# Kernel optimization log

Measured on AMD Instinct MI355X. Metric: run time of the kernel, lower is better.

Reference implementation:

```python
import jax, jax.numpy as jnp
import numpy as np

N_PREV = 8191
DIMS = 4096


def setup_inputs() -> dict:
    key = jax.random.key(0)
    k1, k2, k3, k4, k5 = jax.random.split(key, 5)
    prev_inps = jax.random.normal(k1, (N_PREV, DIMS), dtype=jnp.float32)
    inp = jax.random.normal(k2, (DIMS,), dtype=jnp.float32)
    # learned parameters, init std=0.01 as in the torch module
    W_Q = jax.random.normal(k3, (DIMS, DIMS), dtype=jnp.float32) * 0.01
    W_K = jax.random.normal(k4, (DIMS, DIMS), dtype=jnp.float32) * 0.01
    W_V = jax.random.normal(k5, (DIMS, DIMS), dtype=jnp.float32) * 0.01
    return {"prev_inps": prev_inps, "inp": inp, "W_Q": W_Q, "W_K": W_K, "W_V": W_V}


def reference(prev_inps, inp, W_Q, W_K, W_V):
    # One masked self-attention decode step.
    inputs = jnp.concatenate([prev_inps, inp[None, :]], axis=0)  # (n+1, d)
    query = W_Q @ inp                                            # (d,)
    keys = jnp.einsum('md,nd->nm', W_K, inputs)                  # (n+1, d)
    values = jnp.einsum('md,nd->nm', W_V, inputs)                # (n+1, d)
    logits = keys @ query                                        # (n+1,)
    aweights = jax.nn.softmax(logits, axis=-1)                   # (n+1,)
    context = aweights @ values                                  # (d,)
    output = context + inp                                       # residual
    return (output, inputs)
```

## Files before the change

kernel.cpp:

```cpp
#include <hip/hip_runtime.h>
#include <math.h>

#define D      4096
#define NPREV  8191
#define NROWS  8192

typedef float f4 __attribute__((ext_vector_type(4)));

static __device__ __forceinline__ f4 nt_load4(const float* p) {
    return __builtin_nontemporal_load(reinterpret_cast<const f4*>(p));
}
static __device__ __forceinline__ void nt_store4(f4 v, float* p) {
    __builtin_nontemporal_store(v, reinterpret_cast<f4*>(p));
}
static __device__ __forceinline__ f4 ld4(const float* p) {
    return *reinterpret_cast<const f4*>(p);
}
static __device__ __forceinline__ void st4(f4 v, float* p) {
    *reinterpret_cast<f4*>(p) = v;
}

template<bool RESIDUAL>
__global__ void k_matvec_rows(const float* __restrict__ W, const float* __restrict__ v,
                              const float* __restrict__ resid, float* __restrict__ out) {
    int row  = blockIdx.x * 4 + (threadIdx.x >> 6);
    int lane = threadIdx.x & 63;
    const float* Wrow = W + (size_t)row * D;
    float acc = 0.f;
    #pragma unroll
    for (int i = 0; i < 16; ++i) {
        int c = lane + i * 64;
        f4 w = nt_load4(Wrow + 4 * c);
        f4 x = ld4(v + 4 * c);
        acc += w.x * x.x + w.y * x.y + w.z * x.z + w.w * x.w;
    }
    #pragma unroll
    for (int off = 32; off; off >>= 1) acc += __shfl_down(acc, off, 64);
    if (lane == 0) out[row] = RESIDUAL ? (acc + resid[row]) : acc;
}

#define NCH 64
__global__ void k_colvec_partial(const float* __restrict__ W, const float* __restrict__ q,
                                 float* __restrict__ part) {
    int d4 = blockIdx.x * 256 + threadIdx.x;
    int m0 = blockIdx.y * (D / NCH);
    f4 acc = (f4)0.f;
    #pragma unroll 4
    for (int r = 0; r < D / NCH; ++r) {
        float qm = q[m0 + r];
        acc += qm * nt_load4(W + (size_t)(m0 + r) * D + 4 * d4);
    }
    st4(acc, part + (size_t)blockIdx.y * D + 4 * d4);
}

__global__ void k_kq_reduce(const float* __restrict__ part, float* __restrict__ kq) {
    __shared__ float s[4][64];
    int b = blockIdx.x;
    int cg = threadIdx.x >> 6, l = threadIdx.x & 63;
    float acc = 0.f;
    #pragma unroll
    for (int i = 0; i < NCH / 4; ++i)
        acc += part[(size_t)(cg * (NCH / 4) + i) * D + b * 64 + l];
    s[cg][l] = acc;
    __syncthreads();
    if (cg == 0) kq[b * 64 + l] = s[0][l] + s[1][l] + s[2][l] + s[3][l];
}

#define FB   512
#define FR   (NROWS / FB)
__global__ __launch_bounds__(1024, 4) void k_flash(
        const float* __restrict__ prev, const float* __restrict__ inp,
        const float* __restrict__ kq, float* __restrict__ io,
        float* __restrict__ ms, float* __restrict__ ctxpart) {
    __shared__ float s_wred[16][FR];
    __shared__ float s_log[FR];
    const int n0 = blockIdx.x * FR;
    const int t = threadIdx.x;
    const int wid = t >> 6, lane = t & 63;
    const f4 kqv = ld4(kq + 4 * t);

    f4 x[FR];
    #pragma unroll
    for (int r = 0; r < FR; ++r) {
        int n = n0 + r;
        const float* src = (n < NPREV) ? (prev + (size_t)n * D) : inp;
        x[r] = nt_load4(src + 4 * t);
    }
    float p[FR];
    #pragma unroll
    for (int r = 0; r < FR; ++r) {
        int n = n0 + r;
        nt_store4(x[r], io + (size_t)n * D + 4 * t);
        p[r] = x[r].x * kqv.x + x[r].y * kqv.y + x[r].z * kqv.z + x[r].w * kqv.w;
    }
    #pragma unroll
    for (int r = 0; r < FR; ++r) {
        float v = p[r];
        #pragma unroll
        for (int off = 32; off; off >>= 1) v += __shfl_down(v, off, 64);
        if (lane == 0) s_wred[wid][r] = v;
    }
    __syncthreads();
    if (t < FR) {
        float s = 0.f;
        #pragma unroll
        for (int w = 0; w < 16; ++w) s += s_wred[w][t];
        s_log[t] = s;
    }
    __syncthreads();
    float m_b = -INFINITY;
    #pragma unroll
    for (int r = 0; r < FR; ++r) m_b = fmaxf(m_b, s_log[r]);
    float e[FR], s_b = 0.f;
    #pragma unroll
    for (int r = 0; r < FR; ++r) { e[r] = __expf(s_log[r] - m_b); s_b += e[r]; }
    f4 a = (f4)0.f;
    #pragma unroll
    for (int r = 0; r < FR; ++r) a += e[r] * x[r];
    st4(a, ctxpart + (size_t)blockIdx.x * D + 4 * t);
    if (t == 0) { ms[2 * blockIdx.x] = m_b; ms[2 * blockIdx.x + 1] = s_b; }
}

#define NGRP 32
#define GSZ  (FB / NGRP)
__global__ void k_combine1(const float* __restrict__ ms, const float* __restrict__ ctxpart,
                           float* __restrict__ ctx2, float* __restrict__ msg) {
    __shared__ float sm[2 * GSZ];
    int t = threadIdx.x, g = blockIdx.y;
    if (t < 2 * GSZ) sm[t] = ms[2 * GSZ * g + t];
    __syncthreads();
    float Mg = -INFINITY;
    #pragma unroll
    for (int i = 0; i < GSZ; ++i) Mg = fmaxf(Mg, sm[2 * i]);
    float Sg = 0.f;
    #pragma unroll
    for (int i = 0; i < GSZ; ++i) Sg += sm[2 * i + 1] * __expf(sm[2 * i] - Mg);
    int d4 = blockIdx.x * 256 + t;
    f4 a = (f4)0.f;
    #pragma unroll
    for (int i = 0; i < GSZ; ++i) {
        int b = GSZ * g + i;
        a += __expf(sm[2 * i] - Mg) * ld4(ctxpart + (size_t)b * D + 4 * d4);
    }
    st4(a, ctx2 + (size_t)g * D + 4 * d4);
    if (blockIdx.x == 0 && t == 0) { msg[2 * g] = Mg; msg[2 * g + 1] = Sg; }
}

__global__ void k_combine2(const float* __restrict__ msg, const float* __restrict__ ctx2,
                           float* __restrict__ ctx) {
    __shared__ float sm[2 * NGRP];
    int t = threadIdx.x;
    if (t < 2 * NGRP) sm[t] = msg[t];
    __syncthreads();
    float M = -INFINITY;
    #pragma unroll
    for (int g = 0; g < NGRP; ++g) M = fmaxf(M, sm[2 * g]);
    float S = 0.f;
    #pragma unroll
    for (int g = 0; g < NGRP; ++g) S += sm[2 * g + 1] * __expf(sm[2 * g] - M);
    int d4 = blockIdx.x * 256 + t;
    f4 a = (f4)0.f;
    #pragma unroll
    for (int g = 0; g < NGRP; ++g)
        a += __expf(sm[2 * g] - M) * ld4(ctx2 + (size_t)g * D + 4 * d4);
    st4(a * (1.f / S), ctx + 4 * d4);
}

extern "C" void kernel_launch(void* const* d_in, const int* in_sizes, int n_in,
                              void* d_out, int out_size, void* d_ws, size_t ws_size,
                              hipStream_t stream) {
    const float* prev = (const float*)d_in[0];
    const float* inp  = (const float*)d_in[1];
    const float* W_Q  = (const float*)d_in[2];
    const float* W_K  = (const float*)d_in[3];
    const float* W_V  = (const float*)d_in[4];
    float* out = (float*)d_out;
    float* io  = out + D;
    float* ws  = (float*)d_ws;

    float* q       = ws;
    float* kq      = q + D;
    float* part    = kq + D;
    float* ms      = part + (size_t)NCH * D;
    float* ctxpart = ms + 2 * FB;
    float* ctx2    = ctxpart + (size_t)FB * D;
    float* msg     = ctx2 + (size_t)NGRP * D;
    float* ctx     = msg + 2 * NGRP;

    k_matvec_rows<false><<<1024, 256, 0, stream>>>(W_Q, inp, nullptr, q);
    k_colvec_partial<<<dim3(4, NCH), 256, 0, stream>>>(W_K, q, part);
    k_kq_reduce<<<64, 256, 0, stream>>>(part, kq);
    k_flash<<<FB, 1024, 0, stream>>>(prev, inp, kq, io, ms, ctxpart);
    k_combine1<<<dim3(4, NGRP), 256, 0, stream>>>(ms, ctxpart, ctx2, msg);
    k_combine2<<<4, 256, 0, stream>>>(msg, ctx2, ctx);
    k_matvec_rows<true><<<1024, 256, 0, stream>>>(W_V, ctx, inp, out);
}
```

Before: 121.3 us.

## Fuse reductions into producer kernels via last-block atomic counters

The separate kq reduction kernel is folded into the column-matvec kernel, and the first softmax combine stage is folded into the flash kernel. In each case the last block to finish a group, found with an atomic counter after a threadfence, does the reduction. This removes two kernel launches and their inter-kernel gaps, in exchange for a memset launch, fences and atomics, and a serialized tail where only the last block per group does the reduce.

```diff
diff --git a/kernel.cpp b/kernel.cpp
--- a/kernel.cpp
+++ b/kernel.cpp
@@ -4,6 +4,11 @@
 #define D      4096
 #define NPREV  8191
 #define NROWS  8192
+#define FB     512
+#define FR     (NROWS / FB)
+#define NGRP   32
+#define GSZ    (FB / NGRP)
+#define NCH    64
 
 typedef float f4 __attribute__((ext_vector_type(4)));
 
@@ -39,42 +44,43 @@
     if (lane == 0) out[row] = RESIDUAL ? (acc + resid[row]) : acc;
 }
 
-#define NCH 64
-__global__ void k_colvec_partial(const float* __restrict__ W, const float* __restrict__ q,
-                                 float* __restrict__ part) {
-    int d4 = blockIdx.x * 256 + threadIdx.x;
-    int m0 = blockIdx.y * (D / NCH);
+__global__ void k_kq_fused(const float* __restrict__ W, const float* __restrict__ q,
+                           float* part, float* kq, unsigned int* cnt) {
+    __shared__ int s_flag;
+    int t = threadIdx.x;
+    int s = blockIdx.x;
+    int c = blockIdx.y;
+    int d4 = s * 256 + t;
+    int m0 = c * (D / NCH);
     f4 acc = (f4)0.f;
     #pragma unroll 4
-    for (int r = 0; r < D / NCH; ++r) {
-        float qm = q[m0 + r];
-        acc += qm * nt_load4(W + (size_t)(m0 + r) * D + 4 * d4);
-    }
-    st4(acc, part + (size_t)blockIdx.y * D + 4 * d4);
-}
-
-__global__ void k_kq_reduce(const float* __restrict__ part, float* __restrict__ kq) {
-    __shared__ float s[4][64];
-    int b = blockIdx.x;
-    int cg = threadIdx.x >> 6, l = threadIdx.x & 63;
-    float acc = 0.f;
-    #pragma unroll
-    for (int i = 0; i < NCH / 4; ++i)
-        acc += part[(size_t)(cg * (NCH / 4) + i) * D + b * 64 + l];
-    s[cg][l] = acc;
-    __syncthreads();
-    if (cg == 0) kq[b * 64 + l] = s[0][l] + s[1][l] + s[2][l] + s[3][l];
-}
-
-#define FB   512
-#define FR   (NROWS / FB)
+    for (int r = 0; r < D / NCH; ++r)
+        acc += q[m0 + r] * nt_load4(W + (size_t)(m0 + r) * D + 4 * d4);
+    st4(acc, part + (size_t)c * D + 4 * d4);
+    __threadfence();
+    __syncthreads();
+    if (t == 0) s_flag = (atomicAdd(&cnt[s], 1u) == NCH - 1);
+    __syncthreads();
+    if (s_flag) {
+        __threadfence();
+        f4 a = (f4)0.f;
+        #pragma unroll 8
+        for (int cc = 0; cc < NCH; ++cc)
+            a += ld4(part + (size_t)cc * D + 4 * d4);
+        st4(a, kq + 4 * d4);
+    }
+}
+
 __global__ __launch_bounds__(1024, 4) void k_flash(
         const float* __restrict__ prev, const float* __restrict__ inp,
         const float* __restrict__ kq, float* __restrict__ io,
-        float* __restrict__ ms, float* __restrict__ ctxpart) {
+        float* ms, float* ctxpart, float* ctx2, float* msg, unsigned int* cnt) {
     __shared__ float s_wred[16][FR];
     __shared__ float s_log[FR];
-    const int n0 = blockIdx.x * FR;
+    __shared__ float s_gms[2 * GSZ];
+    __shared__ int s_flag;
+    const int bid = blockIdx.x;
+    const int n0 = bid * FR;
     const int t = threadIdx.x;
     const int wid = t >> 6, lane = t & 63;
     const f4 kqv = ld4(kq + 4 * t);
@@ -117,33 +123,33 @@
     f4 a = (f4)0.f;
     #pragma unroll
     for (int r = 0; r < FR; ++r) a += e[r] * x[r];
-    st4(a, ctxpart + (size_t)blockIdx.x * D + 4 * t);
-    if (t == 0) { ms[2 * blockIdx.x] = m_b; ms[2 * blockIdx.x + 1] = s_b; }
-}
-
-#define NGRP 32
-#define GSZ  (FB / NGRP)
-__global__ void k_combine1(const float* __restrict__ ms, const float* __restrict__ ctxpart,
-                           float* __restrict__ ctx2, float* __restrict__ msg) {
-    __shared__ float sm[2 * GSZ];
-    int t = threadIdx.x, g = blockIdx.y;
-    if (t < 2 * GSZ) sm[t] = ms[2 * GSZ * g + t];
-    __syncthreads();
-    float Mg = -INFINITY;
-    #pragma unroll
-    for (int i = 0; i < GSZ; ++i) Mg = fmaxf(Mg, sm[2 * i]);
-    float Sg = 0.f;
-    #pragma unroll
-    for (int i = 0; i < GSZ; ++i) Sg += sm[2 * i + 1] * __expf(sm[2 * i] - Mg);
-    int d4 = blockIdx.x * 256 + t;
-    f4 a = (f4)0.f;
-    #pragma unroll
-    for (int i = 0; i < GSZ; ++i) {
-        int b = GSZ * g + i;
-        a += __expf(sm[2 * i] - Mg) * ld4(ctxpart + (size_t)b * D + 4 * d4);
-    }
-    st4(a, ctx2 + (size_t)g * D + 4 * d4);
-    if (blockIdx.x == 0 && t == 0) { msg[2 * g] = Mg; msg[2 * g + 1] = Sg; }
+    st4(a, ctxpart + (size_t)bid * D + 4 * t);
+    if (t == 0) { ms[2 * bid] = m_b; ms[2 * bid + 1] = s_b; }
+
+    const int g = bid / GSZ;
+    __threadfence();
+    __syncthreads();
+    if (t == 0) s_flag = (atomicAdd(&cnt[g], 1u) == GSZ - 1);
+    __syncthreads();
+    if (s_flag) {
+        __threadfence();
+        if (t < 2 * GSZ) s_gms[t] = ms[2 * GSZ * g + t];
+        __syncthreads();
+        float Mg = -INFINITY;
+        #pragma unroll
+        for (int i = 0; i < GSZ; ++i) Mg = fmaxf(Mg, s_gms[2 * i]);
+        float Sg = 0.f;
+        #pragma unroll
+        for (int i = 0; i < GSZ; ++i) Sg += s_gms[2 * i + 1] * __expf(s_gms[2 * i] - Mg);
+        f4 ga = (f4)0.f;
+        #pragma unroll
+        for (int i = 0; i < GSZ; ++i) {
+            int b = GSZ * g + i;
+            ga += __expf(s_gms[2 * i] - Mg) * ld4(ctxpart + (size_t)b * D + 4 * t);
+        }
+        st4(ga, ctx2 + (size_t)g * D + 4 * t);
+        if (t == 0) { msg[2 * g] = Mg; msg[2 * g + 1] = Sg; }
+    }
 }
 
 __global__ void k_combine2(const float* __restrict__ msg, const float* __restrict__ ctx2,
@@ -186,12 +192,14 @@
     float* ctx2    = ctxpart + (size_t)FB * D;
     float* msg     = ctx2 + (size_t)NGRP * D;
     float* ctx     = msg + 2 * NGRP;
+    unsigned int* cnt_kq    = (unsigned int*)(ctx + D);
+    unsigned int* cnt_flash = cnt_kq + 4;
+
+    hipMemsetAsync(cnt_kq, 0, (4 + NGRP) * sizeof(unsigned int), stream);
 
     k_matvec_rows<false><<<1024, 256, 0, stream>>>(W_Q, inp, nullptr, q);
-    k_colvec_partial<<<dim3(4, NCH), 256, 0, stream>>>(W_K, q, part);
-    k_kq_reduce<<<64, 256, 0, stream>>>(part, kq);
-    k_flash<<<FB, 1024, 0, stream>>>(prev, inp, kq, io, ms, ctxpart);
-    k_combine1<<<dim3(4, NGRP), 256, 0, stream>>>(ms, ctxpart, ctx2, msg);
+    k_kq_fused<<<dim3(4, NCH), 256, 0, stream>>>(W_K, q, part, kq, cnt_kq);
+    k_flash<<<FB, 1024, 0, stream>>>(prev, inp, kq, io, ms, ctxpart, ctx2, msg, cnt_flash);
     k_combine2<<<4, 256, 0, stream>>>(msg, ctx2, ctx);
     k_matvec_rows<true><<<1024, 256, 0, stream>>>(W_V, ctx, inp, out);
 }
```

Result: slower. 433.3 us (+257.2%).

## Fuse K^T q reduction and softmax combine stages into single kernels

Applied to the files above, without the earlier changes.

Replaces the two-kernel K^T·q computation (partial chunks plus a global reduce) with one kernel that stages q in shared memory and reduces across 64 row groups inside the block. The two-level softmax combine is merged into one kernel that computes the global max and sum per block and then weights all 512 partial contexts. Prev input loads in the flash kernel switch from nontemporal to regular loads. The aim is fewer launches and less intermediate global traffic. The cost is lower parallelism: 256 blocks for kq and 32 blocks for combine.

```diff
diff --git a/kernel.cpp b/kernel.cpp
--- a/kernel.cpp
+++ b/kernel.cpp
@@ -4,6 +4,8 @@
 #define D      4096
 #define NPREV  8191
 #define NROWS  8192
+#define FB     512
+#define FR     (NROWS / FB)
 
 typedef float f4 __attribute__((ext_vector_type(4)));
 
@@ -39,35 +41,32 @@
     if (lane == 0) out[row] = RESIDUAL ? (acc + resid[row]) : acc;
 }
 
-#define NCH 64
-__global__ void k_colvec_partial(const float* __restrict__ W, const float* __restrict__ q,
-                                 float* __restrict__ part) {
-    int d4 = blockIdx.x * 256 + threadIdx.x;
-    int m0 = blockIdx.y * (D / NCH);
+__global__ void k_kq(const float* __restrict__ W, const float* __restrict__ q,
+                     float* __restrict__ kq) {
+    __shared__ float s_q[D];
+    __shared__ f4 s_part[64][4];
+    int t = threadIdx.x;
+    int b = blockIdx.x;
+    for (int i = t; i < D; i += 256) s_q[i] = q[i];
+    __syncthreads();
+    int c4 = b * 4 + (t & 3);
+    int r0 = t >> 2;
     f4 acc = (f4)0.f;
-    #pragma unroll 4
-    for (int r = 0; r < D / NCH; ++r) {
-        float qm = q[m0 + r];
-        acc += qm * nt_load4(W + (size_t)(m0 + r) * D + 4 * d4);
+    #pragma unroll 16
+    for (int i = 0; i < 64; ++i) {
+        int m = r0 + i * 64;
+        acc += s_q[m] * nt_load4(W + (size_t)m * D + 4 * c4);
     }
-    st4(acc, part + (size_t)blockIdx.y * D + 4 * d4);
+    s_part[r0][t & 3] = acc;
+    __syncthreads();
+    if (t < 4) {
+        f4 a = (f4)0.f;
+        #pragma unroll
+        for (int g = 0; g < 64; ++g) a += s_part[g][t];
+        st4(a, kq + 4 * (b * 4 + t));
+    }
 }
 
-__global__ void k_kq_reduce(const float* __restrict__ part, float* __restrict__ kq) {
-    __shared__ float s[4][64];
-    int b = blockIdx.x;
-    int cg = threadIdx.x >> 6, l = threadIdx.x & 63;
-    float acc = 0.f;
-    #pragma unroll
-    for (int i = 0; i < NCH / 4; ++i)
-        acc += part[(size_t)(cg * (NCH / 4) + i) * D + b * 64 + l];
-    s[cg][l] = acc;
-    __syncthreads();
-    if (cg == 0) kq[b * 64 + l] = s[0][l] + s[1][l] + s[2][l] + s[3][l];
-}
-
-#define FB   512
-#define FR   (NROWS / FB)
 __global__ __launch_bounds__(1024, 4) void k_flash(
         const float* __restrict__ prev, const float* __restrict__ inp,
         const float* __restrict__ kq, float* __restrict__ io,
@@ -84,7 +83,7 @@
     for (int r = 0; r < FR; ++r) {
         int n = n0 + r;
         const float* src = (n < NPREV) ? (prev + (size_t)n * D) : inp;
-        x[r] = nt_load4(src + 4 * t);
+        x[r] = ld4(src + 4 * t);
     }
     float p[FR];
     #pragma unroll
@@ -121,49 +120,45 @@
     if (t == 0) { ms[2 * blockIdx.x] = m_b; ms[2 * blockIdx.x + 1] = s_b; }
 }
 
-#define NGRP 32
-#define GSZ  (FB / NGRP)
-__global__ void k_combine1(const float* __restrict__ ms, const float* __restrict__ ctxpart,
-                           float* __restrict__ ctx2, float* __restrict__ msg) {
-    __shared__ float sm[2 * GSZ];
-    int t = threadIdx.x, g = blockIdx.y;
-    if (t < 2 * GSZ) sm[t] = ms[2 * GSZ * g + t];
+__global__ void k_combine(const float* __restrict__ ms, const float* __restrict__ ctxpart,
+                          float* __restrict__ ctx) {
+    __shared__ float s_w[FB];
+    __shared__ float s_red[12];
+    __shared__ f4 s_acc[8][32];
+    int t = threadIdx.x;
+    int lane = t & 63, wid = t >> 6;
+    float m0 = ms[2 * t], m1 = ms[2 * (t + 256)];
+    float mx = fmaxf(m0, m1);
+    #pragma unroll
+    for (int off = 32; off; off >>= 1) mx = fmaxf(mx, __shfl_down(mx, off, 64));
+    if (lane == 0) s_red[wid] = mx;
     __syncthreads();
-    float Mg = -INFINITY;
+    float M = fmaxf(fmaxf(s_red[0], s_red[1]), fmaxf(s_red[2], s_red[3]));
+    float w0 = __expf(m0 - M), w1 = __expf(m1 - M);
+    s_w[t] = w0; s_w[t + 256] = w1;
+    float sc = w0 * ms[2 * t + 1] + w1 * ms[2 * (t + 256) + 1];
     #pragma unroll
-    for (int i = 0; i < GSZ; ++i) Mg = fmaxf(Mg, sm[2 * i]);
-    float Sg = 0.f;
-    #pragma unroll
-    for (int i = 0; i < GSZ; ++i) Sg += sm[2 * i + 1] * __expf(sm[2 * i] - Mg);
-    int d4 = blockIdx.x * 256 + t;
+    for (int off = 32; off; off >>= 1) sc += __shfl_down(sc, off, 64);
+    if (lane == 0) s_red[8 + wid] = sc;
+    __syncthreads();
+    float S = s_red[8] + s_red[9] + s_red[10] + s_red[11];
+    int c  = t & 31;
+    int g8 = t >> 5;
+    int col4 = blockIdx.x * 32 + c;
     f4 a = (f4)0.f;
-    #pragma unroll
-    for (int i = 0; i < GSZ; ++i) {
-        int b = GSZ * g + i;
-        a += __expf(sm[2 * i] - Mg) * ld4(ctxpart + (size_t)b * D + 4 * d4);
+    #pragma unroll 8
+    for (int i = 0; i < 64; ++i) {
+        int p = g8 * 64 + i;
+        a += s_w[p] * ld4(ctxpart + (size_t)p * D + 4 * col4);
     }
-    st4(a, ctx2 + (size_t)g * D + 4 * d4);
-    if (blockIdx.x == 0 && t == 0) { msg[2 * g] = Mg; msg[2 * g + 1] = Sg; }
-}
-
-__global__ void k_combine2(const float* __restrict__ msg, const float* __restrict__ ctx2,
-                           float* __restrict__ ctx) {
-    __shared__ float sm[2 * NGRP];
-    int t = threadIdx.x;
-    if (t < 2 * NGRP) sm[t] = msg[t];
+    s_acc[g8][c] = a;
     __syncthreads();
-    float M = -INFINITY;
-    #pragma unroll
-    for (int g = 0; g < NGRP; ++g) M = fmaxf(M, sm[2 * g]);
-    float S = 0.f;
-    #pragma unroll
-    for (int g = 0; g < NGRP; ++g) S += sm[2 * g + 1] * __expf(sm[2 * g] - M);
-    int d4 = blockIdx.x * 256 + t;
-    f4 a = (f4)0.f;
-    #pragma unroll
-    for (int g = 0; g < NGRP; ++g)
-        a += __expf(sm[2 * g] - M) * ld4(ctx2 + (size_t)g * D + 4 * d4);
-    st4(a * (1.f / S), ctx + 4 * d4);
+    if (t < 32) {
+        f4 aa = (f4)0.f;
+        #pragma unroll
+        for (int g = 0; g < 8; ++g) aa += s_acc[g][t];
+        st4(aa * (1.f / S), ctx + 4 * (blockIdx.x * 32 + t));
+    }
 }
 
 extern "C" void kernel_launch(void* const* d_in, const int* in_sizes, int n_in,
@@ -180,18 +175,13 @@
 
     float* q       = ws;
     float* kq      = q + D;
-    float* part    = kq + D;
-    float* ms      = part + (size_t)NCH * D;
+    float* ms      = kq + D;
     float* ctxpart = ms + 2 * FB;
-    float* ctx2    = ctxpart + (size_t)FB * D;
-    float* msg     = ctx2 + (size_t)NGRP * D;
-    float* ctx     = msg + 2 * NGRP;
+    float* ctx     = ctxpart + (size_t)FB * D;
 
     k_matvec_rows<false><<<1024, 256, 0, stream>>>(W_Q, inp, nullptr, q);
-    k_colvec_partial<<<dim3(4, NCH), 256, 0, stream>>>(W_K, q, part);
-    k_kq_reduce<<<64, 256, 0, stream>>>(part, kq);
+    k_kq<<<256, 256, 0, stream>>>(W_K, q, kq);
     k_flash<<<FB, 1024, 0, stream>>>(prev, inp, kq, io, ms, ctxpart);
-    k_combine1<<<dim3(4, NGRP), 256, 0, stream>>>(ms, ctxpart, ctx2, msg);
-    k_combine2<<<4, 256, 0, stream>>>(msg, ctx2, ctx);
+    k_combine<<<32, 256, 0, stream>>>(ms, ctxpart, ctx);
     k_matvec_rows<true><<<1024, 256, 0, stream>>>(W_V, ctx, inp, out);
 }
```

Result: faster. 116.0 us (-4.4%).
